# Kernel tuning notes

Hardware: AMD Instinct MI355X
Metric: run time of the kernel (lower is better)

Reference implementation:

```python
import jax, jax.numpy as jnp
import numpy as np

N, F, H, G = 8192, 128, 64, 4      # nodes, node_attr_size, hidden_size, num groups
CONV_TH = 1e-05
MAX_ITER = 5


def setup_inputs() -> dict:
    key = jax.random.key(0)
    k1, k2, k3, k4 = jax.random.split(key, 4)
    X = jax.random.normal(k1, (N, F), dtype=jnp.float32)
    # L scaled like a normalized graph operator so the fixed-point is well-behaved
    L = jax.random.normal(k2, (N, N), dtype=jnp.float32) * (1.0 / np.sqrt(N))
    # reservoir weights (requires_grad=False in the original, still materialized here)
    W_ih = jax.random.normal(k3, (G, H, F), dtype=jnp.float32) * (1.0 / np.sqrt(F))
    W_hh = jax.random.normal(k4, (G, H, H), dtype=jnp.float32) * (0.9 / np.sqrt(H))
    return {"X": X, "L": L, "W_ih": W_ih, "W_hh": W_hh}


def _gesn_forward(X, L, W_ih, W_hh):
    # wiu = linear(X, W_ih) per group: [G, N, H]
    wiu = jnp.einsum('nf,ghf->gnh', X, W_ih)
    hx0 = jnp.zeros((G, N, H), dtype=X.dtype)
    done0 = jnp.zeros((G,), dtype=bool)

    def step(carry, _):
        hx, done = carry
        lin = jnp.einsum('gnh,gkh->gnk', hx, W_hh)          # linear(hx, W_hh)
        new = jnp.tanh(wiu + jnp.einsum('nm,gmk->gnk', L, lin))  # mm(L, .) + wiu, tanh activation
        diff = jnp.sqrt(jnp.sum((new - hx) ** 2, axis=(1, 2)))   # ||last_res - res|| per group
        hx_next = jnp.where(done[:, None, None], hx, new)   # masked early-exit (mimics break)
        done = done | (diff < CONV_TH)
        return (hx_next, done), None

    (hx, _), _ = jax.lax.scan(step, (hx0, done0), None, length=MAX_ITER)
    # concat group outputs along feature dim -> [N, G*H]
    return jnp.transpose(hx, (1, 0, 2)).reshape(N, G * H)


def reference(X, L, W_ih, W_hh):
    return _gesn_forward(X, L, W_ih, W_hh)
```

## Files before the change

### kernel.cpp

```cpp
#include <hip/hip_runtime.h>
#include <hip/hip_fp16.h>

#define NN 8192
#define FF 128
#define HH 64
#define GG 4
#define CONV_TH2 1e-10f

typedef _Float16 half8 __attribute__((ext_vector_type(8)));
typedef float floatx4 __attribute__((ext_vector_type(4)));

#define OFF_WIU  134217728ull
#define OFF_LIN  142606336ull
#define OFF_CP   146800640ull
#define OFF_META 180355072ull

__device__ __forceinline__ void load16(const void* g, void* l) {
  __builtin_amdgcn_global_load_lds((const __attribute__((address_space(1))) void*)g,
                                   (__attribute__((address_space(3))) void*)l,
                                   16, 0, 0);
}

__global__ void k_init(float* __restrict__ diffsq, int* __restrict__ done) {
  int t = threadIdx.x;
  if (t < 5 * GG) diffsq[t] = 0.f;
  if (t < GG) done[t] = 0;
}

__global__ void k_done(const float* __restrict__ diffsq, int* __restrict__ done, int it) {
  int t = threadIdx.x;
  if (t < GG) {
    if (diffsq[it * GG + t] < CONV_TH2) done[t] = 1;
  }
}

__global__ __launch_bounds__(256) void k_convert(const float* __restrict__ L,
                                                 _Float16* __restrict__ Lh) {
  size_t i = ((size_t)blockIdx.x * 256 + threadIdx.x) * 8;
  float4 a = *(const float4*)(L + i);
  float4 b = *(const float4*)(L + i + 4);
  half8 h;
  h[0] = (_Float16)a.x; h[1] = (_Float16)a.y; h[2] = (_Float16)a.z; h[3] = (_Float16)a.w;
  h[4] = (_Float16)b.x; h[5] = (_Float16)b.y; h[6] = (_Float16)b.z; h[7] = (_Float16)b.w;
  *(half8*)(Lh + i) = h;
}

__global__ __launch_bounds__(256) void k_wiu(const float* __restrict__ X,
    const float* __restrict__ Wih, const float* __restrict__ Whh,
    float* __restrict__ wiu, float* __restrict__ hx,
    _Float16* __restrict__ lin_t, float* __restrict__ diffsq) {
  __shared__ __align__(16) float smem[2 * 64 * 128];
  float* Xs = smem;
  float* Ws = smem + 64 * 128;
  const int bx = blockIdx.x, g = blockIdx.y;
  const int t = threadIdx.x;
  const int m0 = bx * 64;
  #pragma unroll
  for (int p = 0; p < 8; ++p) {
    int idx = p * 256 + t;
    int row = idx >> 5;
    int c4 = idx & 31;
    int sw = (c4 ^ (row >> 2)) & 31;
    float4 xv = *(const float4*)(X + (size_t)(m0 + row) * FF + c4 * 4);
    *(float4*)(Xs + row * 128 + sw * 4) = xv;
    float4 wv = *(const float4*)(Wih + (size_t)g * HH * FF + (size_t)row * FF + c4 * 4);
    *(float4*)(Ws + row * 128 + sw * 4) = wv;
  }
  __syncthreads();
  const int tc = t & 15, tm = t >> 4;
  float acc[4][4];
  #pragma unroll
  for (int r = 0; r < 4; ++r)
    #pragma unroll
    for (int s = 0; s < 4; ++s) acc[r][s] = 0.f;
  for (int f4 = 0; f4 < 32; ++f4) {
    float4 xv[4], wv[4];
    #pragma unroll
    for (int r = 0; r < 4; ++r) {
      int m = tm * 4 + r;
      xv[r] = *(const float4*)(Xs + m * 128 + (((f4 ^ (m >> 2)) & 31) * 4));
    }
    #pragma unroll
    for (int s = 0; s < 4; ++s) {
      int c = tc * 4 + s;
      wv[s] = *(const float4*)(Ws + c * 128 + (((f4 ^ (c >> 2)) & 31) * 4));
    }
    #pragma unroll
    for (int r = 0; r < 4; ++r)
      #pragma unroll
      for (int s = 0; s < 4; ++s)
        acc[r][s] += xv[r].x * wv[s].x + xv[r].y * wv[s].y +
                     xv[r].z * wv[s].z + xv[r].w * wv[s].w;
  }
  __syncthreads();
  float* hxs = smem;
  float* Whs = smem + 64 * 65;
  float diffp = 0.f;
  #pragma unroll
  for (int r = 0; r < 4; ++r) {
    int ml = tm * 4 + r;
    size_t off = (size_t)(m0 + ml) * 256 + g * 64 + tc * 4;
    float4 wv = make_float4(acc[r][0], acc[r][1], acc[r][2], acc[r][3]);
    *(float4*)(wiu + off) = wv;
    float4 hv;
    hv.x = tanhf(wv.x); hv.y = tanhf(wv.y); hv.z = tanhf(wv.z); hv.w = tanhf(wv.w);
    *(float4*)(hx + off) = hv;
    hxs[ml * 65 + tc * 4 + 0] = hv.x;
    hxs[ml * 65 + tc * 4 + 1] = hv.y;
    hxs[ml * 65 + tc * 4 + 2] = hv.z;
    hxs[ml * 65 + tc * 4 + 3] = hv.w;
    diffp += hv.x * hv.x + hv.y * hv.y + hv.z * hv.z + hv.w * hv.w;
  }
  #pragma unroll
  for (int p = 0; p < 16; ++p) {
    int idx = p * 256 + t;
    Whs[(idx >> 6) * 65 + (idx & 63)] = Whh[(size_t)g * HH * HH + idx];
  }
  for (int o = 32; o; o >>= 1) diffp += __shfl_down(diffp, o);
  if ((t & 63) == 0) atomicAdd(diffsq + g, diffp);
  __syncthreads();
  const int ml = t & 63, wv_ = t >> 6;
  float lacc[16];
  #pragma unroll
  for (int i = 0; i < 16; ++i) lacc[i] = 0.f;
  for (int h = 0; h < 64; ++h) {
    float xh = hxs[ml * 65 + h];
    #pragma unroll
    for (int i = 0; i < 16; ++i)
      lacc[i] += xh * Whs[(wv_ + 4 * i) * 65 + h];
  }
  #pragma unroll
  for (int i = 0; i < 16; ++i)
    lin_t[(size_t)(g * 64 + wv_ + 4 * i) * NN + m0 + ml] = (_Float16)lacc[i];
}

__global__ __launch_bounds__(256) void k_gemm(const _Float16* __restrict__ A,
    const _Float16* __restrict__ Bt, float* __restrict__ Cp) {
  __shared__ __align__(16) _Float16 As[128 * 64];
  __shared__ __align__(16) _Float16 Bs[128 * 64];
  const int bx = blockIdx.x;
  const int by = blockIdx.y;
  const int bz = blockIdx.z;
  const int t = threadIdx.x;
  const int lane = t & 63, wid = t >> 6;
  const int wr = wid >> 1, wc = wid & 1;
  const int l15 = lane & 15, quad = lane >> 4;
  const size_t m0 = (size_t)bx * 128;
  const size_t c0 = (size_t)by * 128;
  const size_t k0 = (size_t)bz * 2048;

  const _Float16* ga[4]; const _Float16* gb[4];
  _Float16* la[4]; _Float16* lb[4];
  #pragma unroll
  for (int i = 0; i < 4; ++i) {
    int ch = i * 256 + t;
    int r = ch >> 3;
    int j = (ch & 7) ^ (r & 7);
    ga[i] = A + (m0 + r) * NN + k0 + j * 8;
    gb[i] = Bt + (c0 + r) * NN + k0 + j * 8;
    la[i] = &As[ch * 8];
    lb[i] = &Bs[ch * 8];
  }
  int aoffs[2][4], boffs[2][4];
  #pragma unroll
  for (int ks = 0; ks < 2; ++ks) {
    #pragma unroll
    for (int mt = 0; mt < 4; ++mt) {
      int m = wr * 64 + mt * 16 + l15;
      aoffs[ks][mt] = m * 64 + (((ks * 4 + quad) ^ (m & 7)) * 8);
    }
    #pragma unroll
    for (int nt = 0; nt < 4; ++nt) {
      int n = wc * 64 + nt * 16 + l15;
      boffs[ks][nt] = n * 64 + (((ks * 4 + quad) ^ (n & 7)) * 8);
    }
  }
  floatx4 acc[4][4];
  #pragma unroll
  for (int mt = 0; mt < 4; ++mt)
    #pragma unroll
    for (int nt = 0; nt < 4; ++nt)
      acc[mt][nt] = (floatx4){0.f, 0.f, 0.f, 0.f};

  for (int rd = 0; rd < 32; ++rd) {
    #pragma unroll
    for (int i = 0; i < 4; ++i) { load16(ga[i], la[i]); load16(gb[i], lb[i]); }
    __syncthreads();
    #pragma unroll
    for (int ks = 0; ks < 2; ++ks) {
      half8 af[4], bf[4];
      #pragma unroll
      for (int mt = 0; mt < 4; ++mt) af[mt] = *(const half8*)&As[aoffs[ks][mt]];
      #pragma unroll
      for (int nt = 0; nt < 4; ++nt) bf[nt] = *(const half8*)&Bs[boffs[ks][nt]];
      #pragma unroll
      for (int mt = 0; mt < 4; ++mt)
        #pragma unroll
        for (int nt = 0; nt < 4; ++nt)
          acc[mt][nt] = __builtin_amdgcn_mfma_f32_16x16x32_f16(af[mt], bf[nt], acc[mt][nt], 0, 0, 0);
    }
    __syncthreads();
    #pragma unroll
    for (int i = 0; i < 4; ++i) { ga[i] += 64; gb[i] += 64; }
  }
  float* Cb = Cp + (size_t)bz * NN * 256;
  #pragma unroll
  for (int mt = 0; mt < 4; ++mt) {
    #pragma unroll
    for (int nt = 0; nt < 4; ++nt) {
      size_t gm = m0 + wr * 64 + mt * 16 + quad * 4;
      size_t gc = c0 + wc * 64 + nt * 16 + l15;
      #pragma unroll
      for (int rg = 0; rg < 4; ++rg)
        Cb[(gm + rg) * 256 + gc] = acc[mt][nt][rg];
    }
  }
}

__global__ __launch_bounds__(256) void k_post(const float* __restrict__ Cp,
    const float* __restrict__ wiu, const float* __restrict__ Whh,
    float* __restrict__ hx, _Float16* __restrict__ lin_t,
    float* __restrict__ diffsq, const int* __restrict__ done,
    int it, int write_lin) {
  __shared__ float hxs[64 * 65];
  __shared__ float Whs[64 * 65];
  const int bx = blockIdx.x, g = blockIdx.y, t = threadIdx.x;
  const int m0 = bx * 64;
  const int tcol = t & 15, trow = t >> 4;
  const int dn = done[g];
  float diffp = 0.f;
  #pragma unroll
  for (int p = 0; p < 4; ++p) {
    int ml = p * 16 + trow;
    size_t off = (size_t)(m0 + ml) * 256 + g * 64 + tcol * 4;
    float4 s  = *(const float4*)(Cp + off);
    float4 q1 = *(const float4*)(Cp + (size_t)1 * NN * 256 + off);
    float4 q2 = *(const float4*)(Cp + (size_t)2 * NN * 256 + off);
    float4 q3 = *(const float4*)(Cp + (size_t)3 * NN * 256 + off);
    s.x += q1.x + q2.x + q3.x; s.y += q1.y + q2.y + q3.y;
    s.z += q1.z + q2.z + q3.z; s.w += q1.w + q2.w + q3.w;
    float4 wv = *(const float4*)(wiu + off);
    float4 old = *(const float4*)(hx + off);
    float4 nv;
    nv.x = tanhf(wv.x + s.x); nv.y = tanhf(wv.y + s.y);
    nv.z = tanhf(wv.z + s.z); nv.w = tanhf(wv.w + s.w);
    float4 ov;
    ov.x = dn ? old.x : nv.x; ov.y = dn ? old.y : nv.y;
    ov.z = dn ? old.z : nv.z; ov.w = dn ? old.w : nv.w;
    *(float4*)(hx + off) = ov;
    float dx = nv.x - old.x, dy = nv.y - old.y, dz = nv.z - old.z, dw = nv.w - old.w;
    diffp += dx * dx + dy * dy + dz * dz + dw * dw;
    hxs[ml * 65 + tcol * 4 + 0] = ov.x;
    hxs[ml * 65 + tcol * 4 + 1] = ov.y;
    hxs[ml * 65 + tcol * 4 + 2] = ov.z;
    hxs[ml * 65 + tcol * 4 + 3] = ov.w;
  }
  if (write_lin) {
    #pragma unroll
    for (int p = 0; p < 16; ++p) {
      int idx = p * 256 + t;
      Whs[(idx >> 6) * 65 + (idx & 63)] = Whh[(size_t)g * HH * HH + idx];
    }
  }
  for (int o = 32; o; o >>= 1) diffp += __shfl_down(diffp, o);
  if ((t & 63) == 0) atomicAdd(diffsq + it * GG + g, diffp);
  if (!write_lin) return;
  __syncthreads();
  const int ml = t & 63, wv_ = t >> 6;
  float lacc[16];
  #pragma unroll
  for (int i = 0; i < 16; ++i) lacc[i] = 0.f;
  for (int h = 0; h < 64; ++h) {
    float xh = hxs[ml * 65 + h];
    #pragma unroll
    for (int i = 0; i < 16; ++i)
      lacc[i] += xh * Whs[(wv_ + 4 * i) * 65 + h];
  }
  #pragma unroll
  for (int i = 0; i < 16; ++i)
    lin_t[(size_t)(g * 64 + wv_ + 4 * i) * NN + m0 + ml] = (_Float16)lacc[i];
}

extern "C" void kernel_launch(void* const* d_in, const int* in_sizes, int n_in,
                              void* d_out, int out_size, void* d_ws, size_t ws_size,
                              hipStream_t stream) {
  const float* X   = (const float*)d_in[0];
  const float* L   = (const float*)d_in[1];
  const float* Wih = (const float*)d_in[2];
  const float* Whh = (const float*)d_in[3];
  float* out = (float*)d_out;
  char* ws = (char*)d_ws;
  _Float16* Lh    = (_Float16*)ws;
  float*    wiu   = (float*)(ws + OFF_WIU);
  _Float16* lin_t = (_Float16*)(ws + OFF_LIN);
  float*    Cp    = (float*)(ws + OFF_CP);
  float*    diffsq = (float*)(ws + OFF_META);
  int*      done   = (int*)(ws + OFF_META + 128);

  k_init<<<1, 64, 0, stream>>>(diffsq, done);
  k_convert<<<32768, 256, 0, stream>>>(L, Lh);
  k_wiu<<<dim3(128, 4), 256, 0, stream>>>(X, Wih, Whh, wiu, out, lin_t, diffsq);
  k_done<<<1, 64, 0, stream>>>(diffsq, done, 0);
  for (int it = 1; it <= 4; ++it) {
    k_gemm<<<dim3(64, 2, 4), 256, 0, stream>>>(Lh, lin_t, Cp);
    k_post<<<dim3(128, 4), 256, 0, stream>>>(Cp, wiu, Whh, out, lin_t, diffsq, done,
                                             it, (it < 4) ? 1 : 0);
    k_done<<<1, 64, 0, stream>>>(diffsq, done, it);
  }
}
```

Baseline: 762.3 us.

## Shrink GEMM M-tile to 64 rows and fold convergence checks into post kernel

The split-K GEMM tile moves from 128x128 to 64x128. This doubles the block count to 1024 and reorders the grid so the two column blocks that share an A row tile run next to each other, which should improve occupancy and L2 reuse of the fp16 L matrix. The tiny init and done kernels are removed. diffsq is zeroed inside the convert kernel, and the post kernel works out the done flag from earlier diffsq entries, cutting 6 launches. The cost is that each block reuses its B tile over fewer rows, so more LDS traffic is spent per MFMA.

Result: slower. 804.1 us (+5.5%).

```diff
diff --git a/kernel.cpp b/kernel.cpp
--- a/kernel.cpp
+++ b/kernel.cpp
@@ -21,21 +21,10 @@
                                    16, 0, 0);
 }
 
-__global__ void k_init(float* __restrict__ diffsq, int* __restrict__ done) {
-  int t = threadIdx.x;
-  if (t < 5 * GG) diffsq[t] = 0.f;
-  if (t < GG) done[t] = 0;
-}
-
-__global__ void k_done(const float* __restrict__ diffsq, int* __restrict__ done, int it) {
-  int t = threadIdx.x;
-  if (t < GG) {
-    if (diffsq[it * GG + t] < CONV_TH2) done[t] = 1;
-  }
-}
-
 __global__ __launch_bounds__(256) void k_convert(const float* __restrict__ L,
-                                                 _Float16* __restrict__ Lh) {
+                                                 _Float16* __restrict__ Lh,
+                                                 float* __restrict__ diffsq) {
+  if (blockIdx.x == 0 && threadIdx.x < 5 * GG) diffsq[threadIdx.x] = 0.f;
   size_t i = ((size_t)blockIdx.x * 256 + threadIdx.x) * 8;
   float4 a = *(const float4*)(L + i);
   float4 b = *(const float4*)(L + i + 4);
@@ -136,37 +125,43 @@
 
 __global__ __launch_bounds__(256) void k_gemm(const _Float16* __restrict__ A,
     const _Float16* __restrict__ Bt, float* __restrict__ Cp) {
-  __shared__ __align__(16) _Float16 As[128 * 64];
+  __shared__ __align__(16) _Float16 As[64 * 64];
   __shared__ __align__(16) _Float16 Bs[128 * 64];
-  const int bx = blockIdx.x;
-  const int by = blockIdx.y;
+  const int by = blockIdx.x;
+  const int bx = blockIdx.y;
   const int bz = blockIdx.z;
   const int t = threadIdx.x;
   const int lane = t & 63, wid = t >> 6;
-  const int wr = wid >> 1, wc = wid & 1;
+  const int wr = wid & 1, wc = wid >> 1;
   const int l15 = lane & 15, quad = lane >> 4;
-  const size_t m0 = (size_t)bx * 128;
+  const size_t m0 = (size_t)bx * 64;
   const size_t c0 = (size_t)by * 128;
   const size_t k0 = (size_t)bz * 2048;
 
-  const _Float16* ga[4]; const _Float16* gb[4];
-  _Float16* la[4]; _Float16* lb[4];
+  const _Float16* ga[2]; _Float16* la[2];
+  #pragma unroll
+  for (int i = 0; i < 2; ++i) {
+    int ch = i * 256 + t;
+    int r = ch >> 3;
+    int j = (ch & 7) ^ (r & 7);
+    ga[i] = A + (m0 + r) * NN + k0 + j * 8;
+    la[i] = &As[ch * 8];
+  }
+  const _Float16* gb[4]; _Float16* lb[4];
   #pragma unroll
   for (int i = 0; i < 4; ++i) {
     int ch = i * 256 + t;
     int r = ch >> 3;
     int j = (ch & 7) ^ (r & 7);
-    ga[i] = A + (m0 + r) * NN + k0 + j * 8;
     gb[i] = Bt + (c0 + r) * NN + k0 + j * 8;
-    la[i] = &As[ch * 8];
     lb[i] = &Bs[ch * 8];
   }
-  int aoffs[2][4], boffs[2][4];
+  int aoffs[2][2], boffs[2][4];
   #pragma unroll
   for (int ks = 0; ks < 2; ++ks) {
     #pragma unroll
-    for (int mt = 0; mt < 4; ++mt) {
-      int m = wr * 64 + mt * 16 + l15;
+    for (int mt = 0; mt < 2; ++mt) {
+      int m = wr * 32 + mt * 16 + l15;
       aoffs[ks][mt] = m * 64 + (((ks * 4 + quad) ^ (m & 7)) * 8);
     }
     #pragma unroll
@@ -175,40 +170,44 @@
       boffs[ks][nt] = n * 64 + (((ks * 4 + quad) ^ (n & 7)) * 8);
     }
   }
-  floatx4 acc[4][4];
-  #pragma unroll
-  for (int mt = 0; mt < 4; ++mt)
+  floatx4 acc[2][4];
+  #pragma unroll
+  for (int mt = 0; mt < 2; ++mt)
     #pragma unroll
     for (int nt = 0; nt < 4; ++nt)
       acc[mt][nt] = (floatx4){0.f, 0.f, 0.f, 0.f};
 
   for (int rd = 0; rd < 32; ++rd) {
     #pragma unroll
-    for (int i = 0; i < 4; ++i) { load16(ga[i], la[i]); load16(gb[i], lb[i]); }
+    for (int i = 0; i < 2; ++i) load16(ga[i], la[i]);
+    #pragma unroll
+    for (int i = 0; i < 4; ++i) load16(gb[i], lb[i]);
     __syncthreads();
     #pragma unroll
     for (int ks = 0; ks < 2; ++ks) {
-      half8 af[4], bf[4];
-      #pragma unroll
-      for (int mt = 0; mt < 4; ++mt) af[mt] = *(const half8*)&As[aoffs[ks][mt]];
+      half8 af[2], bf[4];
+      #pragma unroll
+      for (int mt = 0; mt < 2; ++mt) af[mt] = *(const half8*)&As[aoffs[ks][mt]];
       #pragma unroll
       for (int nt = 0; nt < 4; ++nt) bf[nt] = *(const half8*)&Bs[boffs[ks][nt]];
       #pragma unroll
-      for (int mt = 0; mt < 4; ++mt)
+      for (int mt = 0; mt < 2; ++mt)
         #pragma unroll
         for (int nt = 0; nt < 4; ++nt)
           acc[mt][nt] = __builtin_amdgcn_mfma_f32_16x16x32_f16(af[mt], bf[nt], acc[mt][nt], 0, 0, 0);
     }
     __syncthreads();
     #pragma unroll
-    for (int i = 0; i < 4; ++i) { ga[i] += 64; gb[i] += 64; }
+    for (int i = 0; i < 2; ++i) ga[i] += 64;
+    #pragma unroll
+    for (int i = 0; i < 4; ++i) gb[i] += 64;
   }
   float* Cb = Cp + (size_t)bz * NN * 256;
   #pragma unroll
-  for (int mt = 0; mt < 4; ++mt) {
+  for (int mt = 0; mt < 2; ++mt) {
     #pragma unroll
     for (int nt = 0; nt < 4; ++nt) {
-      size_t gm = m0 + wr * 64 + mt * 16 + quad * 4;
+      size_t gm = m0 + wr * 32 + mt * 16 + quad * 4;
       size_t gc = c0 + wc * 64 + nt * 16 + l15;
       #pragma unroll
       for (int rg = 0; rg < 4; ++rg)
@@ -220,14 +219,16 @@
 __global__ __launch_bounds__(256) void k_post(const float* __restrict__ Cp,
     const float* __restrict__ wiu, const float* __restrict__ Whh,
     float* __restrict__ hx, _Float16* __restrict__ lin_t,
-    float* __restrict__ diffsq, const int* __restrict__ done,
-    int it, int write_lin) {
+    float* __restrict__ diffsq, int it, int write_lin) {
   __shared__ float hxs[64 * 65];
   __shared__ float Whs[64 * 65];
   const int bx = blockIdx.x, g = blockIdx.y, t = threadIdx.x;
   const int m0 = bx * 64;
   const int tcol = t & 15, trow = t >> 4;
-  const int dn = done[g];
+  int dn = 0;
+  #pragma unroll
+  for (int j = 0; j < 4; ++j)
+    if (j < it && diffsq[j * GG + g] < CONV_TH2) dn = 1;
   float diffp = 0.f;
   #pragma unroll
   for (int p = 0; p < 4; ++p) {
@@ -295,16 +296,12 @@
   _Float16* lin_t = (_Float16*)(ws + OFF_LIN);
   float*    Cp    = (float*)(ws + OFF_CP);
   float*    diffsq = (float*)(ws + OFF_META);
-  int*      done   = (int*)(ws + OFF_META + 128);
-
-  k_init<<<1, 64, 0, stream>>>(diffsq, done);
-  k_convert<<<32768, 256, 0, stream>>>(L, Lh);
+
+  k_convert<<<32768, 256, 0, stream>>>(L, Lh, diffsq);
   k_wiu<<<dim3(128, 4), 256, 0, stream>>>(X, Wih, Whh, wiu, out, lin_t, diffsq);
-  k_done<<<1, 64, 0, stream>>>(diffsq, done, 0);
   for (int it = 1; it <= 4; ++it) {
-    k_gemm<<<dim3(64, 2, 4), 256, 0, stream>>>(Lh, lin_t, Cp);
-    k_post<<<dim3(128, 4), 256, 0, stream>>>(Cp, wiu, Whh, out, lin_t, diffsq, done,
+    k_gemm<<<dim3(2, 128, 4), 256, 0, stream>>>(Lh, lin_t, Cp);
+    k_post<<<dim3(128, 4), 256, 0, stream>>>(Cp, wiu, Whh, out, lin_t, diffsq,
                                              it, (it < 4) ? 1 : 0);
-    k_done<<<1, 64, 0, stream>>>(diffsq, done, it);
-  }
-}
+  }
+}
```
